# Kernel optimization log

Hardware: AMD Instinct MI355X
Metric: run time of the kernel (lower is better)

Reference implementation:

```python
import jax, jax.numpy as jnp
import numpy as np

B, S, D_IN, RANK, D_OUT = 8, 1024, 1280, 64, 1280
DOWN_SIZE = RANK * D_IN      # 81920
UP_SIZE = D_OUT * RANK       # 81920


def setup_inputs() -> dict:
    key = jax.random.key(0)
    k1, k2 = jax.random.split(key)
    x = jax.random.normal(k1, (B, S, D_IN), dtype=jnp.float32)
    # per-image embedding that encodes the dynamic LoRA weights
    embed = jax.random.normal(k2, (B, DOWN_SIZE + UP_SIZE), dtype=jnp.float32) * 0.02
    return {"x": x, "embed": embed}


def reference(x, embed):
    # down_forward: per-sample weight = embed[:, :down_size].view(down_shape)=[rank, d_in]
    # original does x_chunk @ W.T per sample; batched as a single grouped GEMM
    w_down = embed[:, :DOWN_SIZE].reshape(B, RANK, D_IN)   # [B, r, d_in]
    h = jnp.einsum('bsd,brd->bsr', x, w_down)              # x @ W_down.T, batched
    # up_forward: per-sample weight = embed[:, -up_size:].view(up_shape)=[d_out, rank]
    w_up = embed[:, -UP_SIZE:].reshape(B, D_OUT, RANK)     # [B, d_out, r]
    out = jnp.einsum('bsr,bor->bso', h, w_up)              # h @ W_up.T, batched
    return out
```

## Files before the change

### kernel.cpp

```cpp
#include <hip/hip_runtime.h>

#define NB   8
#define S_   1024
#define DIN  1280
#define RANK 64
#define DOUT 1280
#define DOWN (RANK * DIN)
#define EMB  (DOWN + DOUT * RANK)
#define XSTRIDE 1288

#define XLS_OFF   0
#define XLS_BYTES (16 * XSTRIDE * 2)
#define WB_OFF    XLS_BYTES
#define WB_BYTES  (2 * 16384)
#define PB_OFF    (WB_OFF + WB_BYTES)
#define PB_BYTES  (4 * 16 * 17 * 4)
#define HL_OFF    (PB_OFF + PB_BYTES)
#define HL_BYTES  (16 * 80 * 2)
#define LDS_TOTAL (HL_OFF + HL_BYTES)

typedef __bf16 bf16x8 __attribute__((ext_vector_type(8)));
typedef __bf16 bf16x4 __attribute__((ext_vector_type(4)));
typedef float  f32x4  __attribute__((ext_vector_type(4)));

#define GLOAD16(gsrc, ldsoff)                                              \
    __builtin_amdgcn_global_load_lds(                                      \
        (const __attribute__((address_space(1))) void*)(gsrc),             \
        (__attribute__((address_space(3))) void*)(smem + (ldsoff)),        \
        16, 0, 0)

__global__ __launch_bounds__(256) void cvt_embed(const float* __restrict__ src,
                                                 __bf16* __restrict__ dst, int n8) {
    const int i = blockIdx.x * 256 + threadIdx.x;
    if (i < n8) {
        const float4* s = reinterpret_cast<const float4*>(src) + (size_t)i * 2;
        float4 f0 = s[0], f1 = s[1];
        bf16x8 v;
        v[0]=(__bf16)f0.x; v[1]=(__bf16)f0.y; v[2]=(__bf16)f0.z; v[3]=(__bf16)f0.w;
        v[4]=(__bf16)f1.x; v[5]=(__bf16)f1.y; v[6]=(__bf16)f1.z; v[7]=(__bf16)f1.w;
        *reinterpret_cast<bf16x8*>(dst + (size_t)i * 8) = v;
    }
}

__global__ __launch_bounds__(512, 2) void lora_main(const float* __restrict__ x,
                                                    const __bf16* __restrict__ ew,
                                                    float* __restrict__ out) {
    extern __shared__ char smem[];
    __bf16* xls = (__bf16*)(smem + XLS_OFF);
    float (*pbuf)[16][17] = (float(*)[16][17])(smem + PB_OFF);
    __bf16 (*hld)[80]     = (__bf16(*)[80])(smem + HL_OFF);

    const int b    = blockIdx.x & 7;
    const int s0   = (blockIdx.x >> 3) * 16;
    const int t    = threadIdx.x;
    const int w    = t >> 6;
    const int l    = t & 63;
    const int quad = l >> 4;
    const int lc   = l & 15;
    const int dq   = quad * 8;

    const int nt = w & 3;
    const int kh = w >> 2;

    const char* wdB = (const char*)(ew + (size_t)b * EMB);
    const char* wuB = wdB + (size_t)DOWN * 2;
    const int d0 = w * 2048 + l * 16;
    const int d1 = d0 + 1024;
    const int kh0 = d0 >> 13,        kh1 = d1 >> 13;
    const int r0  = (d0 >> 7) & 63,  r1  = (d1 >> 7) & 63;
    const int cB0 = d0 & 127,        cB1 = d1 & 127;
    const char* p1a = wdB + r0 * 2560 + kh0 * 1280 + (cB0 ^ ((r0 & 7) << 4));
    const char* p1b = wdB + r1 * 2560 + kh1 * 1280 + (cB1 ^ ((r1 & 7) << 4));
    const char* p2a = wuB + (d0 ^ (((d0 >> 7) & 7) << 4));
    const char* p2b = wuB + (d1 ^ (((d1 >> 7) & 7) << 4));
    const int ldsA = WB_OFF + w * 2048;
    const int bswz = (lc & 7) << 4;

    GLOAD16(p1a, ldsA);
    GLOAD16(p1b, ldsA + 1024);
    {
        const int row = t >> 5;
        const int c   = t & 31;
        const float4* src = reinterpret_cast<const float4*>(x + (size_t)(b * S_ + s0 + row) * DIN);
        __bf16* drow = xls + row * XSTRIDE;
#pragma unroll
        for (int j = 0; j < 10; ++j) {
            float4 f = src[c + 32 * j];
            bf16x4 v;
            v[0]=(__bf16)f.x; v[1]=(__bf16)f.y; v[2]=(__bf16)f.z; v[3]=(__bf16)f.w;
            *reinterpret_cast<bf16x4*>(drow + c * 4 + 128 * j) = v;
        }
    }
    __syncthreads();

    const __bf16* xrow = xls + lc * XSTRIDE + kh * 640;
    const int brow = kh * 8192 + (nt * 16 + lc) * 128;
    f32x4 acc = {0,0,0,0};
#pragma unroll
    for (int c = 0; c < 10; ++c) {
        const int nb = (c & 1) ^ 1;
        if (c < 9) {
            GLOAD16(p1a + (c + 1) * 128, nb * 16384 + ldsA);
            GLOAD16(p1b + (c + 1) * 128, nb * 16384 + ldsA + 1024);
        } else {
            GLOAD16(p2a, ldsA);
            GLOAD16(p2b, ldsA + 1024);
        }
        const char* bb = smem + WB_OFF + (c & 1) * 16384;
#pragma unroll
        for (int j = 0; j < 2; ++j) {
            bf16x8 af = *reinterpret_cast<const bf16x8*>(xrow + c * 64 + j * 32 + dq);
            bf16x8 bf = *reinterpret_cast<const bf16x8*>(bb + ((brow + j * 64 + quad * 16) ^ bswz));
            acc = __builtin_amdgcn_mfma_f32_16x16x32_bf16(af, bf, acc, 0, 0, 0);
        }
        __syncthreads();
    }

    if (kh == 1) {
#pragma unroll
        for (int i = 0; i < 4; ++i) pbuf[nt][quad * 4 + i][lc] = acc[i];
    }
    __syncthreads();
    if (kh == 0) {
#pragma unroll
        for (int i = 0; i < 4; ++i) {
            float v = acc[i] + pbuf[nt][quad * 4 + i][lc];
            hld[quad * 4 + i][nt * 16 + lc] = (__bf16)v;
        }
    }
    __syncthreads();

    bf16x8 ha0 = *reinterpret_cast<const bf16x8*>(&hld[lc][dq]);
    bf16x8 ha1 = *reinterpret_cast<const bf16x8*>(&hld[lc][32 + dq]);
    float* obase = out + (size_t)(b * S_ + s0 + quad * 4) * DOUT;
    const int prow = (w * 16 + lc) * 128;

#pragma unroll
    for (int tt = 0; tt < 10; ++tt) {
        if (tt < 9) {
            const int nb = (tt & 1) ^ 1;
            GLOAD16(p2a + (tt + 1) * 16384, nb * 16384 + ldsA);
            GLOAD16(p2b + (tt + 1) * 16384, nb * 16384 + ldsA + 1024);
        }
        const char* bb = smem + WB_OFF + (tt & 1) * 16384;
        bf16x8 b0 = *reinterpret_cast<const bf16x8*>(bb + ((prow + quad * 16) ^ bswz));
        bf16x8 b1 = *reinterpret_cast<const bf16x8*>(bb + ((prow + 64 + quad * 16) ^ bswz));
        f32x4 c4 = {0,0,0,0};
        c4 = __builtin_amdgcn_mfma_f32_16x16x32_bf16(ha0, b0, c4, 0, 0, 0);
        c4 = __builtin_amdgcn_mfma_f32_16x16x32_bf16(ha1, b1, c4, 0, 0, 0);
        const int o = (w + 8 * tt) * 16 + lc;
#pragma unroll
        for (int i = 0; i < 4; ++i)
            obase[(size_t)i * DOUT + o] = c4[i];
        if (tt < 9) __syncthreads();
    }
}

extern "C" void kernel_launch(void* const* d_in, const int* in_sizes, int n_in,
                              void* d_out, int out_size, void* d_ws, size_t ws_size,
                              hipStream_t stream) {
    const float* x     = (const float*)d_in[0];
    const float* embed = (const float*)d_in[1];
    float*       out   = (float*)d_out;
    __bf16*      ew    = (__bf16*)d_ws;
    (void)in_sizes; (void)n_in; (void)out_size; (void)ws_size;

    cvt_embed<<<dim3(640), dim3(256), 0, stream>>>(embed, ew, NB * EMB / 8);
    lora_main<<<dim3(512), dim3(512), LDS_TOTAL, stream>>>(x, ew, out);
}
```

Before: 100.3 us.

## Fuse embed fp32-to-bf16 conversion into main LoRA kernel, dropping separate pass

Removes the standalone cvt_embed kernel. The main kernel now streams fp32 LoRA weights directly from the embedding into LDS and converts them to bf16 at MFMA operand load, with chunking doubled (20 half-size steps) to fit the same LDS buffers. This drops a kernel launch and a write/read of the bf16 workspace. In exchange, every block reads twice as many bytes of weights and does redundant per-block conversion with more barriers. The x loads are also batched before conversion.

```diff
diff --git a/kernel.cpp b/kernel.cpp
--- a/kernel.cpp
+++ b/kernel.cpp
@@ -9,7 +9,6 @@
 #define EMB  (DOWN + DOUT * RANK)
 #define XSTRIDE 1288
 
-#define XLS_OFF   0
 #define XLS_BYTES (16 * XSTRIDE * 2)
 #define WB_OFF    XLS_BYTES
 #define WB_BYTES  (2 * 16384)
@@ -23,30 +22,24 @@
 typedef __bf16 bf16x4 __attribute__((ext_vector_type(4)));
 typedef float  f32x4  __attribute__((ext_vector_type(4)));
 
+__device__ __forceinline__ bf16x8 cvt8(float4 f0, float4 f1) {
+    bf16x8 v;
+    v[0]=(__bf16)f0.x; v[1]=(__bf16)f0.y; v[2]=(__bf16)f0.z; v[3]=(__bf16)f0.w;
+    v[4]=(__bf16)f1.x; v[5]=(__bf16)f1.y; v[6]=(__bf16)f1.z; v[7]=(__bf16)f1.w;
+    return v;
+}
+
 #define GLOAD16(gsrc, ldsoff)                                              \
     __builtin_amdgcn_global_load_lds(                                      \
         (const __attribute__((address_space(1))) void*)(gsrc),             \
         (__attribute__((address_space(3))) void*)(smem + (ldsoff)),        \
         16, 0, 0)
 
-__global__ __launch_bounds__(256) void cvt_embed(const float* __restrict__ src,
-                                                 __bf16* __restrict__ dst, int n8) {
-    const int i = blockIdx.x * 256 + threadIdx.x;
-    if (i < n8) {
-        const float4* s = reinterpret_cast<const float4*>(src) + (size_t)i * 2;
-        float4 f0 = s[0], f1 = s[1];
-        bf16x8 v;
-        v[0]=(__bf16)f0.x; v[1]=(__bf16)f0.y; v[2]=(__bf16)f0.z; v[3]=(__bf16)f0.w;
-        v[4]=(__bf16)f1.x; v[5]=(__bf16)f1.y; v[6]=(__bf16)f1.z; v[7]=(__bf16)f1.w;
-        *reinterpret_cast<bf16x8*>(dst + (size_t)i * 8) = v;
-    }
-}
-
-__global__ __launch_bounds__(512, 2) void lora_main(const float* __restrict__ x,
-                                                    const __bf16* __restrict__ ew,
-                                                    float* __restrict__ out) {
+__global__ __launch_bounds__(512, 2) void lora_fused(const float* __restrict__ x,
+                                                     const float* __restrict__ embed,
+                                                     float* __restrict__ out) {
     extern __shared__ char smem[];
-    __bf16* xls = (__bf16*)(smem + XLS_OFF);
+    __bf16* xls = (__bf16*)smem;
     float (*pbuf)[16][17] = (float(*)[16][17])(smem + PB_OFF);
     __bf16 (*hld)[80]     = (__bf16(*)[80])(smem + HL_OFF);
 
@@ -62,57 +55,58 @@
     const int nt = w & 3;
     const int kh = w >> 2;
 
-    const char* wdB = (const char*)(ew + (size_t)b * EMB);
-    const char* wuB = wdB + (size_t)DOWN * 2;
+    const char* eb  = (const char*)(embed + (size_t)b * EMB);
+    const char* wub = eb + (size_t)DOWN * 4;
+
     const int d0 = w * 2048 + l * 16;
     const int d1 = d0 + 1024;
-    const int kh0 = d0 >> 13,        kh1 = d1 >> 13;
-    const int r0  = (d0 >> 7) & 63,  r1  = (d1 >> 7) & 63;
-    const int cB0 = d0 & 127,        cB1 = d1 & 127;
-    const char* p1a = wdB + r0 * 2560 + kh0 * 1280 + (cB0 ^ ((r0 & 7) << 4));
-    const char* p1b = wdB + r1 * 2560 + kh1 * 1280 + (cB1 ^ ((r1 & 7) << 4));
-    const char* p2a = wuB + (d0 ^ (((d0 >> 7) & 7) << 4));
-    const char* p2b = wuB + (d1 ^ (((d1 >> 7) & 7) << 4));
+    const int kA = d0 >> 13,        kB = d1 >> 13;
+    const int rA = (d0 >> 7) & 63,  rB = (d1 >> 7) & 63;
+    const int cA = d0 & 127,        cB = d1 & 127;
+    const char* p1a = eb + rA * 5120 + kA * 2560 + (cA ^ ((rA & 7) << 4));
+    const char* p1b = eb + rB * 5120 + kB * 2560 + (cB ^ ((rB & 7) << 4));
+    const int r2A = d0 >> 7,        r2B = d1 >> 7;
+    const char* p2a = wub + r2A * 256 + ((d0 & 127) ^ ((r2A & 7) << 4));
+    const char* p2b = wub + r2B * 256 + ((d1 & 127) ^ ((r2B & 7) << 4));
     const int ldsA = WB_OFF + w * 2048;
-    const int bswz = (lc & 7) << 4;
 
     GLOAD16(p1a, ldsA);
     GLOAD16(p1b, ldsA + 1024);
     {
         const int row = t >> 5;
-        const int c   = t & 31;
+        const int cc  = t & 31;
         const float4* src = reinterpret_cast<const float4*>(x + (size_t)(b * S_ + s0 + row) * DIN);
+        float4 f[10];
+#pragma unroll
+        for (int j = 0; j < 10; ++j) f[j] = src[cc + 32 * j];
         __bf16* drow = xls + row * XSTRIDE;
 #pragma unroll
         for (int j = 0; j < 10; ++j) {
-            float4 f = src[c + 32 * j];
             bf16x4 v;
-            v[0]=(__bf16)f.x; v[1]=(__bf16)f.y; v[2]=(__bf16)f.z; v[3]=(__bf16)f.w;
-            *reinterpret_cast<bf16x4*>(drow + c * 4 + 128 * j) = v;
+            v[0]=(__bf16)f[j].x; v[1]=(__bf16)f[j].y; v[2]=(__bf16)f[j].z; v[3]=(__bf16)f[j].w;
+            *reinterpret_cast<bf16x4*>(drow + cc * 4 + 128 * j) = v;
         }
     }
     __syncthreads();
 
     const __bf16* xrow = xls + lc * XSTRIDE + kh * 640;
-    const int brow = kh * 8192 + (nt * 16 + lc) * 128;
+    const int brd = kh * 8192 + (nt * 16 + lc) * 128 + quad * 32;
+    const int sw  = (lc & 7) << 4;
     f32x4 acc = {0,0,0,0};
 #pragma unroll
-    for (int c = 0; c < 10; ++c) {
-        const int nb = (c & 1) ^ 1;
-        if (c < 9) {
-            GLOAD16(p1a + (c + 1) * 128, nb * 16384 + ldsA);
-            GLOAD16(p1b + (c + 1) * 128, nb * 16384 + ldsA + 1024);
+    for (int c = 0; c < 20; ++c) {
+        if (c < 19) {
+            GLOAD16(p1a + (c + 1) * 128, ((c + 1) & 1) * 16384 + ldsA);
+            GLOAD16(p1b + (c + 1) * 128, ((c + 1) & 1) * 16384 + ldsA + 1024);
         } else {
             GLOAD16(p2a, ldsA);
             GLOAD16(p2b, ldsA + 1024);
         }
         const char* bb = smem + WB_OFF + (c & 1) * 16384;
-#pragma unroll
-        for (int j = 0; j < 2; ++j) {
-            bf16x8 af = *reinterpret_cast<const bf16x8*>(xrow + c * 64 + j * 32 + dq);
-            bf16x8 bf = *reinterpret_cast<const bf16x8*>(bb + ((brow + j * 64 + quad * 16) ^ bswz));
-            acc = __builtin_amdgcn_mfma_f32_16x16x32_bf16(af, bf, acc, 0, 0, 0);
-        }
+        bf16x8 af = *reinterpret_cast<const bf16x8*>(xrow + c * 32 + dq);
+        float4 w0 = *reinterpret_cast<const float4*>(bb + (brd ^ sw));
+        float4 w1 = *reinterpret_cast<const float4*>(bb + ((brd + 16) ^ sw));
+        acc = __builtin_amdgcn_mfma_f32_16x16x32_bf16(af, cvt8(w0, w1), acc, 0, 0, 0);
         __syncthreads();
     }
 
@@ -133,26 +127,29 @@
     bf16x8 ha0 = *reinterpret_cast<const bf16x8*>(&hld[lc][dq]);
     bf16x8 ha1 = *reinterpret_cast<const bf16x8*>(&hld[lc][32 + dq]);
     float* obase = out + (size_t)(b * S_ + s0 + quad * 4) * DOUT;
-    const int prow = (w * 16 + lc) * 128;
+    const int rr  = w * 16 + lc;
+    const int prd = rr * 128 + quad * 32;
 
+    f32x4 c4 = {0,0,0,0};
 #pragma unroll
-    for (int tt = 0; tt < 10; ++tt) {
-        if (tt < 9) {
-            const int nb = (tt & 1) ^ 1;
-            GLOAD16(p2a + (tt + 1) * 16384, nb * 16384 + ldsA);
-            GLOAD16(p2b + (tt + 1) * 16384, nb * 16384 + ldsA + 1024);
+    for (int t2 = 0; t2 < 20; ++t2) {
+        if (t2 < 19) {
+            const int nx = t2 + 1;
+            GLOAD16(p2a + (nx >> 1) * 32768 + (nx & 1) * 128, (nx & 1) * 16384 + ldsA);
+            GLOAD16(p2b + (nx >> 1) * 32768 + (nx & 1) * 128, (nx & 1) * 16384 + ldsA + 1024);
         }
-        const char* bb = smem + WB_OFF + (tt & 1) * 16384;
-        bf16x8 b0 = *reinterpret_cast<const bf16x8*>(bb + ((prow + quad * 16) ^ bswz));
-        bf16x8 b1 = *reinterpret_cast<const bf16x8*>(bb + ((prow + 64 + quad * 16) ^ bswz));
-        f32x4 c4 = {0,0,0,0};
-        c4 = __builtin_amdgcn_mfma_f32_16x16x32_bf16(ha0, b0, c4, 0, 0, 0);
-        c4 = __builtin_amdgcn_mfma_f32_16x16x32_bf16(ha1, b1, c4, 0, 0, 0);
-        const int o = (w + 8 * tt) * 16 + lc;
+        const char* bb = smem + WB_OFF + (t2 & 1) * 16384;
+        float4 w0 = *reinterpret_cast<const float4*>(bb + (prd ^ sw));
+        float4 w1 = *reinterpret_cast<const float4*>(bb + ((prd + 16) ^ sw));
+        c4 = __builtin_amdgcn_mfma_f32_16x16x32_bf16((t2 & 1) ? ha1 : ha0, cvt8(w0, w1), c4, 0, 0, 0);
+        if (t2 & 1) {
+            const int o = (t2 >> 1) * 128 + rr;
 #pragma unroll
-        for (int i = 0; i < 4; ++i)
-            obase[(size_t)i * DOUT + o] = c4[i];
-        if (tt < 9) __syncthreads();
+            for (int i = 0; i < 4; ++i)
+                obase[(size_t)i * DOUT + o] = c4[i];
+            c4[0]=0.f; c4[1]=0.f; c4[2]=0.f; c4[3]=0.f;
+        }
+        if (t2 < 19) __syncthreads();
     }
 }
 
@@ -162,9 +159,7 @@
     const float* x     = (const float*)d_in[0];
     const float* embed = (const float*)d_in[1];
     float*       out   = (float*)d_out;
-    __bf16*      ew    = (__bf16*)d_ws;
-    (void)in_sizes; (void)n_in; (void)out_size; (void)ws_size;
+    (void)in_sizes; (void)n_in; (void)out_size; (void)d_ws; (void)ws_size;
 
-    cvt_embed<<<dim3(640), dim3(256), 0, stream>>>(embed, ew, NB * EMB / 8);
-    lora_main<<<dim3(512), dim3(512), LDS_TOTAL, stream>>>(x, ew, out);
+    lora_fused<<<dim3(512), dim3(512), LDS_TOTAL, stream>>>(x, embed, out);
 }
```

After: 114.5 us. 14.1% more time.
